# Kernel tuning notes

Hardware: AMD Instinct MI355X
Metric: run time of the kernel (lower is better)

Reference implementation:

```python
import jax, jax.numpy as jnp
import numpy as np

N_NODES = 50000
BN_EPS = 1e-5
L2_EPS = 1e-12


def setup_inputs() -> dict:
    key = jax.random.key(0)
    k_h, k_w, k_s, k_d = jax.random.split(key, 4)
    h = jax.random.normal(k_h, (N_NODES, 128), dtype=jnp.float32)
    W = jax.random.normal(k_w, (128, 128), dtype=jnp.float32) * (1.0 / np.sqrt(128))
    gamma = jnp.ones((128,), dtype=jnp.float32)
    beta = jnp.zeros((128,), dtype=jnp.float32)
    src = jax.random.randint(k_s, (600000,), 0, N_NODES, dtype=jnp.int64 if jax.config.jax_enable_x64 else jnp.int32)
    dst = jax.random.randint(k_d, (600000,), 0, N_NODES, dtype=jnp.int64 if jax.config.jax_enable_x64 else jnp.int32)
    return {"h": h, "W": W, "gamma": gamma, "beta": beta, "src": src, "dst": dst}


def reference(h, W, gamma, beta, src, dst):
    N = h.shape[0]
    ones = jnp.ones(src.shape[0], dtype=h.dtype)
    # degrees, clamped to >= 1 (DGL GraphConv norm='both')
    deg_out = jnp.clip(jax.ops.segment_sum(ones, src, num_segments=N), 1.0)
    deg_in = jnp.clip(jax.ops.segment_sum(ones, dst, num_segments=N), 1.0)
    # src-side normalization
    hn = h * jax.lax.rsqrt(deg_out)[:, None]
    # gather-scatter aggregation over edges (sum of src messages at dst)
    agg = jax.ops.segment_sum(hn[src], dst, num_segments=N)  # [N, dim_in]
    # dst-side normalization, then linear (in_feats <= out_feats branch)
    agg = agg * jax.lax.rsqrt(deg_in)[:, None]
    out = agg @ W  # [N, dim_out]
    # BatchNorm1d (training-mode batch stats, biased variance)
    mu = jnp.mean(out, axis=0)
    var = jnp.mean(jnp.square(out - mu), axis=0)
    out = (out - mu) * jax.lax.rsqrt(var + BN_EPS) * gamma + beta
    # ReLU
    out = jax.nn.relu(out)
    # F.normalize(p=2, dim=1)
    norm = jnp.sqrt(jnp.sum(jnp.square(out), axis=1, keepdims=True))
    out = out / jnp.maximum(norm, L2_EPS)
    return out
```

## Files before the change

### kernel.cpp

```cpp
#include <hip/hip_runtime.h>
#include <hip/hip_bf16.h>

#define N_NODES 50000
#define N_EDGES 600000
#define SLOTS 64
#define GEMM_BLOCKS 782
#define GATHER_BLOCKS 3125
#define NPART 3125
#define RED_BLOCKS 125

#define Z_OFF        0ull
#define ESRCP_OFF    12800000ull
#define CURS_OFF     25600000ull
#define DEGO_OFF     25800000ull
#define ZERO_OFF     25600000ull
#define ZERO_BYTES   400000ull
#define FLAG_OFF     26000064ull
#define WSW_OFF      26000128ull
#define PSUM_OFF     26032896ull
#define PSQ_OFF      27632896ull
#define PS2_OFF      29232896ull
#define PQ2_OFF      29296896ull
#define SCALE_OFF    29360896ull
#define SHIFT_OFF    29361408ull
#define OUTPRE_OFF   33554432ull
#define HN_OFF       46354432ull

typedef short bf16x8 __attribute__((ext_vector_type(8)));
typedef float f32x4  __attribute__((ext_vector_type(4)));

__device__ __forceinline__ float bf16lo(unsigned int v) { return __uint_as_float(v << 16); }
__device__ __forceinline__ float bf16hi(unsigned int v) { return __uint_as_float(v & 0xffff0000u); }
__device__ __forceinline__ unsigned int packbf16(float x, float y) {
  union { __hip_bfloat162 v; unsigned int u; } cvt;
  cvt.v.x = __float2bfloat16(x);
  cvt.v.y = __float2bfloat16(y);
  return cvt.u;
}

__global__ __launch_bounds__(256) void k_build(const int* __restrict__ src,
                                               const int* __restrict__ dst,
                                               int* __restrict__ cursor,
                                               int* __restrict__ dego,
                                               int* __restrict__ esrcPad,
                                               const unsigned int* __restrict__ hu,
                                               int* __restrict__ flag) {
  __shared__ int cnt;
  if (blockIdx.x == 0) {
    if (threadIdx.x == 0) cnt = 0;
    __syncthreads();
    unsigned int u = hu[threadIdx.x];
    int ex = (u >> 7) & 0xFF;
    if (ex >= 100 && ex <= 140) atomicAdd(&cnt, 1);
    __syncthreads();
    if (threadIdx.x == 0) *flag = (cnt >= 128) ? 1 : 0;
  }
  int e = blockIdx.x * 256 + threadIdx.x;
  if (e < N_EDGES) {
    int s = src[e];
    int d = dst[e];
    atomicAdd(&dego[s], 1);
    int slot = atomicAdd(&cursor[d], 1);
    if (slot < SLOTS) esrcPad[d * SLOTS + slot] = s;
  }
}

__global__ __launch_bounds__(256) void k_prep(const void* __restrict__ hraw,
                                              const int* __restrict__ dego,
                                              const int* __restrict__ flag,
                                              unsigned int* __restrict__ hn,
                                              const void* __restrict__ Wraw,
                                              unsigned int* __restrict__ wsw) {
  int isbf = *flag;
  if (blockIdx.x < 32) {
    int i = blockIdx.x * 256 + threadIdx.x;
    int tileIdx = i >> 8;
    int rem     = i & 255;
    int ln      = rem >> 2;
    int dw      = rem & 3;
    int kb      = tileIdx & 3;
    int ct      = tileIdx >> 2;
    int q       = ln >> 4;
    int n       = ln & 15;
    int k       = kb * 32 + q * 8 + dw * 2;
    int c       = ct * 16 + n;
    unsigned int val;
    if (isbf) {
      const unsigned int* Wd = (const unsigned int*)Wraw;
      unsigned int u0 = Wd[k * 64 + (c >> 1)];
      unsigned int u1 = Wd[(k + 1) * 64 + (c >> 1)];
      unsigned int h0 = (c & 1) ? (u0 >> 16) : (u0 & 0xffffu);
      unsigned int h1 = (c & 1) ? (u1 >> 16) : (u1 & 0xffffu);
      val = h0 | (h1 << 16);
    } else {
      const float* Wf = (const float*)Wraw;
      val = packbf16(Wf[k * 128 + c], Wf[(k + 1) * 128 + c]);
    }
    wsw[i] = val;
  }
  int nn = blockIdx.x * 4 + (threadIdx.x >> 6);
  int l = threadIdx.x & 63;
  float c = rsqrtf((float)max(dego[nn], 1));
  unsigned int out;
  if (isbf) {
    unsigned int v = ((const unsigned int*)hraw)[(size_t)nn * 64 + l];
    out = packbf16(bf16lo(v) * c, bf16hi(v) * c);
  } else {
    float2 v = ((const float2*)hraw)[(size_t)nn * 64 + l];
    out = packbf16(v.x * c, v.y * c);
  }
  hn[(size_t)nn * 64 + l] = out;
}

__global__ __launch_bounds__(256) void k_gemmZ(const unsigned int* __restrict__ hn,
                                               const unsigned int* __restrict__ wsw,
                                               __hip_bfloat16* __restrict__ Z) {
  __shared__ uint4 lb4[2048];
  __shared__ unsigned int la[64 * 68];
  unsigned int* lb = (unsigned int*)lb4;
  int t = threadIdx.x;
  int r0 = blockIdx.x * 64;

  for (int i = t; i < 2048; i += 256) lb4[i] = ((const uint4*)wsw)[i];
  for (int i = t; i < 1024; i += 256) {
    int row  = i >> 4;
    int dpos = (i & 15) * 4;
    int r    = r0 + row;
    uint4 v;
    if (r < N_NODES) v = *(const uint4*)&hn[(size_t)r * 64 + dpos];
    else             v = make_uint4(0u, 0u, 0u, 0u);
    *(uint4*)&la[row * 68 + dpos] = v;
  }
  __syncthreads();

  int l = t & 63;
  int w = t >> 6;
  int m = l & 15;
  int q = l >> 4;

  f32x4 acc[8];
#pragma unroll
  for (int ct = 0; ct < 8; ++ct) acc[ct] = (f32x4){0.f, 0.f, 0.f, 0.f};

#pragma unroll
  for (int kb = 0; kb < 4; ++kb) {
    bf16x8 af = *(const bf16x8*)&la[(w * 16 + m) * 68 + kb * 16 + q * 4];
#pragma unroll
    for (int ct = 0; ct < 8; ++ct) {
      bf16x8 bfv = *(const bf16x8*)&lb[(ct * 4 + kb) * 256 + l * 4];
      acc[ct] = __builtin_amdgcn_mfma_f32_16x16x32_bf16(af, bfv, acc[ct], 0, 0, 0);
    }
  }

#pragma unroll
  for (int ct = 0; ct < 8; ++ct) {
    int col = ct * 16 + m;
#pragma unroll
    for (int reg = 0; reg < 4; ++reg) {
      int row = r0 + w * 16 + q * 4 + reg;
      if (row < N_NODES) Z[(size_t)row * 128 + col] = __float2bfloat16(acc[ct][reg]);
    }
  }
}

__global__ __launch_bounds__(256) void k_gatherZ(const unsigned int* __restrict__ Zd,
                                                 const int* __restrict__ cursor,
                                                 const int* __restrict__ esrcPad,
                                                 unsigned int* __restrict__ outpre,
                                                 float* __restrict__ psum,
                                                 float* __restrict__ psq) {
  __shared__ float sred[4 * 128];
  int t = threadIdx.x;
  int w = t >> 6;
  int l = t & 63;
  float s1a = 0.f, s1b = 0.f, s2a = 0.f, s2b = 0.f;
#pragma unroll
  for (int i = 0; i < 4; ++i) {
    int n = blockIdx.x * 16 + w * 4 + i;
    int di = cursor[n];
    int cnt = di < SLOTS ? di : SLOTS;
    const int* row = esrcPad + n * SLOTS;
    float a0 = 0.f, a1 = 0.f;
    int j = 0;
    for (; j + 3 < cnt; j += 4) {
      int4 s4 = *(const int4*)&row[j];
      unsigned int v0 = Zd[(size_t)s4.x * 64 + l];
      unsigned int v1 = Zd[(size_t)s4.y * 64 + l];
      unsigned int v2 = Zd[(size_t)s4.z * 64 + l];
      unsigned int v3 = Zd[(size_t)s4.w * 64 + l];
      a0 += bf16lo(v0) + bf16lo(v1) + bf16lo(v2) + bf16lo(v3);
      a1 += bf16hi(v0) + bf16hi(v1) + bf16hi(v2) + bf16hi(v3);
    }
    for (; j < cnt; ++j) {
      unsigned int v = Zd[(size_t)row[j] * 64 + l];
      a0 += bf16lo(v);
      a1 += bf16hi(v);
    }
    float scn = rsqrtf((float)(di < 1 ? 1 : di));
    a0 *= scn; a1 *= scn;
    outpre[(size_t)n * 64 + l] = packbf16(a0, a1);
    s1a += a0; s2a += a0 * a0;
    s1b += a1; s2b += a1 * a1;
  }
  sred[w * 128 + 2 * l]     = s1a;
  sred[w * 128 + 2 * l + 1] = s1b;
  __syncthreads();
  if (t < 128) {
    float v = sred[t] + sred[128 + t] + sred[256 + t] + sred[384 + t];
    psum[(size_t)blockIdx.x * 128 + t] = v;
  }
  __syncthreads();
  sred[w * 128 + 2 * l]     = s2a;
  sred[w * 128 + 2 * l + 1] = s2b;
  __syncthreads();
  if (t < 128) {
    float v = sred[t] + sred[128 + t] + sred[256 + t] + sred[384 + t];
    psq[(size_t)blockIdx.x * 128 + t] = v;
  }
}

__global__ __launch_bounds__(256) void k_bnred(const float* __restrict__ psum,
                                               const float* __restrict__ psq,
                                               float* __restrict__ ps2,
                                               float* __restrict__ pq2) {
  __shared__ float r1[256], r2[256];
  int t = threadIdx.x;
  int c = t & 127;
  int j = t >> 7;
  int b0 = blockIdx.x * 25;
  float s1 = 0.f, s2 = 0.f;
  for (int b = b0 + j; b < b0 + 25; b += 2) {
    s1 += psum[(size_t)b * 128 + c];
    s2 += psq [(size_t)b * 128 + c];
  }
  r1[t] = s1; r2[t] = s2;
  __syncthreads();
  if (j == 0) {
    ps2[(size_t)blockIdx.x * 128 + c] = s1 + r1[c + 128];
    pq2[(size_t)blockIdx.x * 128 + c] = s2 + r2[c + 128];
  }
}

__global__ __launch_bounds__(1024) void k_bnfinal(const float* __restrict__ ps2,
                                                  const float* __restrict__ pq2,
                                                  const void* __restrict__ gamma,
                                                  const void* __restrict__ beta,
                                                  const int* __restrict__ flag,
                                                  float* __restrict__ scale,
                                                  float* __restrict__ shift) {
  __shared__ float r1[1024], r2[1024];
  int t = threadIdx.x;
  int c = t & 127;
  int j = t >> 7;
  float s1 = 0.f, s2 = 0.f;
  for (int b = j; b < RED_BLOCKS; b += 8) {
    s1 += ps2[(size_t)b * 128 + c];
    s2 += pq2[(size_t)b * 128 + c];
  }
  r1[t] = s1; r2[t] = s2;
  __syncthreads();
  if (j == 0) {
#pragma unroll
    for (int jj = 1; jj < 8; ++jj) { s1 += r1[c + 128 * jj]; s2 += r2[c + 128 * jj]; }
    const float invN = 1.0f / (float)N_NODES;
    float mu  = s1 * invN;
    float var = s2 * invN - mu * mu;
    float is  = rsqrtf(var + 1e-5f);
    float g, b;
    if (*flag) {
      g = __bfloat162float(((const __hip_bfloat16*)gamma)[c]);
      b = __bfloat162float(((const __hip_bfloat16*)beta)[c]);
    } else {
      g = ((const float*)gamma)[c];
      b = ((const float*)beta)[c];
    }
    scale[c] = g * is;
    shift[c] = b - mu * g * is;
  }
}

__global__ __launch_bounds__(256) void k_rownorm(const unsigned int* __restrict__ outpre,
                                                 const float* __restrict__ scale,
                                                 const float* __restrict__ shift,
                                                 const int* __restrict__ flag,
                                                 void* __restrict__ outraw) {
  int r = blockIdx.x * 4 + (threadIdx.x >> 6);
  int l = threadIdx.x & 63;
  unsigned int xv = outpre[(size_t)r * 64 + l];
  float2 sc = *(const float2*)&scale[2 * l];
  float2 sh = *(const float2*)&shift[2 * l];
  float y0 = fmaxf(bf16lo(xv) * sc.x + sh.x, 0.f);
  float y1 = fmaxf(bf16hi(xv) * sc.y + sh.y, 0.f);
  float ss = y0 * y0 + y1 * y1;
#pragma unroll
  for (int o = 1; o < 64; o <<= 1) ss += __shfl_xor(ss, o, 64);
  float inv = 1.0f / fmaxf(sqrtf(ss), 1e-12f);
  y0 *= inv; y1 *= inv;
  if (*flag) {
    ((unsigned int*)outraw)[(size_t)r * 64 + l] = packbf16(y0, y1);
  } else {
    float2 o2; o2.x = y0; o2.y = y1;
    ((float2*)outraw)[(size_t)r * 64 + l] = o2;
  }
}

extern "C" void kernel_launch(void* const* d_in, const int* in_sizes, int n_in,
                              void* d_out, int out_size, void* d_ws, size_t ws_size,
                              hipStream_t stream) {
  const void* h     = d_in[0];
  const void* W     = d_in[1];
  const void* gamma = d_in[2];
  const void* beta  = d_in[3];
  const int*  src   = (const int*)d_in[4];
  const int*  dst   = (const int*)d_in[5];

  char* ws = (char*)d_ws;
  unsigned int* Zd   = (unsigned int*)(ws + Z_OFF);
  int*   esrcPad = (int*)(ws + ESRCP_OFF);
  int*   cursor  = (int*)(ws + CURS_OFF);
  int*   dego    = (int*)(ws + DEGO_OFF);
  int*   flag    = (int*)(ws + FLAG_OFF);
  unsigned int* wsw = (unsigned int*)(ws + WSW_OFF);
  float* psum    = (float*)(ws + PSUM_OFF);
  float* psq     = (float*)(ws + PSQ_OFF);
  float* ps2     = (float*)(ws + PS2_OFF);
  float* pq2     = (float*)(ws + PQ2_OFF);
  float* scale   = (float*)(ws + SCALE_OFF);
  float* shift   = (float*)(ws + SHIFT_OFF);
  unsigned int* outpre = (unsigned int*)(ws + OUTPRE_OFF);
  unsigned int* hn     = (unsigned int*)(ws + HN_OFF);

  (void)hipMemsetAsync(ws + ZERO_OFF, 0, ZERO_BYTES, stream);

  hipLaunchKernelGGL(k_build, dim3((N_EDGES + 255) / 256), dim3(256), 0, stream,
                     src, dst, cursor, dego, esrcPad, (const unsigned int*)h, flag);
  hipLaunchKernelGGL(k_prep, dim3(N_NODES / 4), dim3(256), 0, stream,
                     h, dego, flag, hn, W, wsw);
  hipLaunchKernelGGL(k_gemmZ, dim3(GEMM_BLOCKS), dim3(256), 0, stream,
                     hn, wsw, (__hip_bfloat16*)Zd);
  hipLaunchKernelGGL(k_gatherZ, dim3(GATHER_BLOCKS), dim3(256), 0, stream,
                     Zd, cursor, esrcPad, outpre, psum, psq);
  hipLaunchKernelGGL(k_bnred, dim3(RED_BLOCKS), dim3(256), 0, stream,
                     psum, psq, ps2, pq2);
  hipLaunchKernelGGL(k_bnfinal, dim3(1), dim3(1024), 0, stream,
                     ps2, pq2, gamma, beta, flag, scale, shift);
  hipLaunchKernelGGL(k_rownorm, dim3(N_NODES / 4), dim3(256), 0, stream,
                     outpre, scale, shift, flag, (unsigned int*)d_out);
}
```

Measured before the change: 216.4 us.

## Fuse prep into build and GEMM, move BN partial stats into reduction kernel

The W swizzle moves into extra blocks of the edge-build kernel, and the degree scaling and bf16 conversion of h move into the GEMM's tile load, so the separate prep kernel and the hn buffer go away. The gather kernel no longer computes per-block BN partial sums. Instead k_bnred reads the bf16 outpre back and reduces it per 400-row chunk. This saves one launch and the hn write/read, at the cost of re-reading outpre (about 12.8MB) for the statistics. The stats are now computed from bf16-rounded values, a small precision change.

```diff
diff --git a/kernel.cpp b/kernel.cpp
--- a/kernel.cpp
+++ b/kernel.cpp
@@ -4,9 +4,9 @@
 #define N_NODES 50000
 #define N_EDGES 600000
 #define SLOTS 64
+#define EDGE_BLOCKS 2344
 #define GEMM_BLOCKS 782
 #define GATHER_BLOCKS 3125
-#define NPART 3125
 #define RED_BLOCKS 125
 
 #define Z_OFF        0ull
@@ -17,14 +17,11 @@
 #define ZERO_BYTES   400000ull
 #define FLAG_OFF     26000064ull
 #define WSW_OFF      26000128ull
-#define PSUM_OFF     26032896ull
-#define PSQ_OFF      27632896ull
-#define PS2_OFF      29232896ull
-#define PQ2_OFF      29296896ull
-#define SCALE_OFF    29360896ull
-#define SHIFT_OFF    29361408ull
+#define PS2_OFF      26032896ull
+#define PQ2_OFF      26096896ull
+#define SCALE_OFF    26160896ull
+#define SHIFT_OFF    26161408ull
 #define OUTPRE_OFF   33554432ull
-#define HN_OFF       46354432ull
 
 typedef short bf16x8 __attribute__((ext_vector_type(8)));
 typedef float f32x4  __attribute__((ext_vector_type(4)));
@@ -44,36 +41,20 @@
                                                int* __restrict__ dego,
                                                int* __restrict__ esrcPad,
                                                const unsigned int* __restrict__ hu,
-                                               int* __restrict__ flag) {
-  __shared__ int cnt;
-  if (blockIdx.x == 0) {
-    if (threadIdx.x == 0) cnt = 0;
+                                               int* __restrict__ flag,
+                                               const void* __restrict__ Wraw,
+                                               unsigned int* __restrict__ wsw) {
+  int t = threadIdx.x;
+  if (blockIdx.x >= EDGE_BLOCKS) {
+    __shared__ int cnt;
+    if (t == 0) cnt = 0;
     __syncthreads();
-    unsigned int u = hu[threadIdx.x];
+    unsigned int u = hu[t];
     int ex = (u >> 7) & 0xFF;
     if (ex >= 100 && ex <= 140) atomicAdd(&cnt, 1);
     __syncthreads();
-    if (threadIdx.x == 0) *flag = (cnt >= 128) ? 1 : 0;
-  }
-  int e = blockIdx.x * 256 + threadIdx.x;
-  if (e < N_EDGES) {
-    int s = src[e];
-    int d = dst[e];
-    atomicAdd(&dego[s], 1);
-    int slot = atomicAdd(&cursor[d], 1);
-    if (slot < SLOTS) esrcPad[d * SLOTS + slot] = s;
-  }
-}
-
-__global__ __launch_bounds__(256) void k_prep(const void* __restrict__ hraw,
-                                              const int* __restrict__ dego,
-                                              const int* __restrict__ flag,
-                                              unsigned int* __restrict__ hn,
-                                              const void* __restrict__ Wraw,
-                                              unsigned int* __restrict__ wsw) {
-  int isbf = *flag;
-  if (blockIdx.x < 32) {
-    int i = blockIdx.x * 256 + threadIdx.x;
+    int isbf = (cnt >= 128);
+    int i = (blockIdx.x - EDGE_BLOCKS) * 256 + t;
     int tileIdx = i >> 8;
     int rem     = i & 255;
     int ln      = rem >> 2;
@@ -97,22 +78,31 @@
       val = packbf16(Wf[k * 128 + c], Wf[(k + 1) * 128 + c]);
     }
     wsw[i] = val;
-  }
-  int nn = blockIdx.x * 4 + (threadIdx.x >> 6);
-  int l = threadIdx.x & 63;
-  float c = rsqrtf((float)max(dego[nn], 1));
-  unsigned int out;
-  if (isbf) {
-    unsigned int v = ((const unsigned int*)hraw)[(size_t)nn * 64 + l];
-    out = packbf16(bf16lo(v) * c, bf16hi(v) * c);
-  } else {
-    float2 v = ((const float2*)hraw)[(size_t)nn * 64 + l];
-    out = packbf16(v.x * c, v.y * c);
-  }
-  hn[(size_t)nn * 64 + l] = out;
-}
-
-__global__ __launch_bounds__(256) void k_gemmZ(const unsigned int* __restrict__ hn,
+    return;
+  }
+  if (blockIdx.x == 0) {
+    __shared__ int cnt0;
+    if (t == 0) cnt0 = 0;
+    __syncthreads();
+    unsigned int u = hu[t];
+    int ex = (u >> 7) & 0xFF;
+    if (ex >= 100 && ex <= 140) atomicAdd(&cnt0, 1);
+    __syncthreads();
+    if (t == 0) *flag = (cnt0 >= 128) ? 1 : 0;
+  }
+  int e = blockIdx.x * 256 + t;
+  if (e < N_EDGES) {
+    int s = src[e];
+    int d = dst[e];
+    atomicAdd(&dego[s], 1);
+    int slot = atomicAdd(&cursor[d], 1);
+    if (slot < SLOTS) esrcPad[d * SLOTS + slot] = s;
+  }
+}
+
+__global__ __launch_bounds__(256) void k_gemmZ(const void* __restrict__ hraw,
+                                               const int* __restrict__ dego,
+                                               const int* __restrict__ flag,
                                                const unsigned int* __restrict__ wsw,
                                                __hip_bfloat16* __restrict__ Z) {
   __shared__ uint4 lb4[2048];
@@ -120,16 +110,34 @@
   unsigned int* lb = (unsigned int*)lb4;
   int t = threadIdx.x;
   int r0 = blockIdx.x * 64;
+  int isbf = *flag;
 
   for (int i = t; i < 2048; i += 256) lb4[i] = ((const uint4*)wsw)[i];
   for (int i = t; i < 1024; i += 256) {
     int row  = i >> 4;
     int dpos = (i & 15) * 4;
     int r    = r0 + row;
-    uint4 v;
-    if (r < N_NODES) v = *(const uint4*)&hn[(size_t)r * 64 + dpos];
-    else             v = make_uint4(0u, 0u, 0u, 0u);
-    *(uint4*)&la[row * 68 + dpos] = v;
+    unsigned int o0 = 0, o1 = 0, o2 = 0, o3 = 0;
+    if (r < N_NODES) {
+      float c = rsqrtf((float)max(dego[r], 1));
+      if (isbf) {
+        uint4 v = *(const uint4*)&((const unsigned int*)hraw)[(size_t)r * 64 + dpos];
+        o0 = packbf16(bf16lo(v.x) * c, bf16hi(v.x) * c);
+        o1 = packbf16(bf16lo(v.y) * c, bf16hi(v.y) * c);
+        o2 = packbf16(bf16lo(v.z) * c, bf16hi(v.z) * c);
+        o3 = packbf16(bf16lo(v.w) * c, bf16hi(v.w) * c);
+      } else {
+        const float* hF = (const float*)hraw;
+        float4 a = *(const float4*)&hF[(size_t)r * 128 + dpos * 2];
+        float4 b = *(const float4*)&hF[(size_t)r * 128 + dpos * 2 + 4];
+        o0 = packbf16(a.x * c, a.y * c);
+        o1 = packbf16(a.z * c, a.w * c);
+        o2 = packbf16(b.x * c, b.y * c);
+        o3 = packbf16(b.z * c, b.w * c);
+      }
+    }
+    unsigned int* p = &la[row * 68 + dpos];
+    p[0] = o0; p[1] = o1; p[2] = o2; p[3] = o3;
   }
   __syncthreads();
 
@@ -166,14 +174,10 @@
 __global__ __launch_bounds__(256) void k_gatherZ(const unsigned int* __restrict__ Zd,
                                                  const int* __restrict__ cursor,
                                                  const int* __restrict__ esrcPad,
-                                                 unsigned int* __restrict__ outpre,
-                                                 float* __restrict__ psum,
-                                                 float* __restrict__ psq) {
-  __shared__ float sred[4 * 128];
+                                                 unsigned int* __restrict__ outpre) {
   int t = threadIdx.x;
   int w = t >> 6;
   int l = t & 63;
-  float s1a = 0.f, s1b = 0.f, s2a = 0.f, s2b = 0.f;
 #pragma unroll
   for (int i = 0; i < 4; ++i) {
     int n = blockIdx.x * 16 + w * 4 + i;
@@ -197,47 +201,37 @@
       a1 += bf16hi(v);
     }
     float scn = rsqrtf((float)(di < 1 ? 1 : di));
-    a0 *= scn; a1 *= scn;
-    outpre[(size_t)n * 64 + l] = packbf16(a0, a1);
-    s1a += a0; s2a += a0 * a0;
-    s1b += a1; s2b += a1 * a1;
+    outpre[(size_t)n * 64 + l] = packbf16(a0 * scn, a1 * scn);
+  }
+}
+
+__global__ __launch_bounds__(256) void k_bnred(const unsigned int* __restrict__ outpre,
+                                               float* __restrict__ ps2,
+                                               float* __restrict__ pq2) {
+  __shared__ float sred[4 * 128];
+  int t = threadIdx.x;
+  int w = t >> 6;
+  int l = t & 63;
+  int r0 = blockIdx.x * 400;
+  float s1a = 0.f, s1b = 0.f, s2a = 0.f, s2b = 0.f;
+  for (int r = r0 + w; r < r0 + 400; r += 4) {
+    unsigned int v = outpre[(size_t)r * 64 + l];
+    float x0 = bf16lo(v), x1 = bf16hi(v);
+    s1a += x0; s2a += x0 * x0;
+    s1b += x1; s2b += x1 * x1;
   }
   sred[w * 128 + 2 * l]     = s1a;
   sred[w * 128 + 2 * l + 1] = s1b;
   __syncthreads();
   if (t < 128) {
-    float v = sred[t] + sred[128 + t] + sred[256 + t] + sred[384 + t];
-    psum[(size_t)blockIdx.x * 128 + t] = v;
+    ps2[(size_t)blockIdx.x * 128 + t] = sred[t] + sred[128 + t] + sred[256 + t] + sred[384 + t];
   }
   __syncthreads();
   sred[w * 128 + 2 * l]     = s2a;
   sred[w * 128 + 2 * l + 1] = s2b;
   __syncthreads();
   if (t < 128) {
-    float v = sred[t] + sred[128 + t] + sred[256 + t] + sred[384 + t];
-    psq[(size_t)blockIdx.x * 128 + t] = v;
-  }
-}
-
-__global__ __launch_bounds__(256) void k_bnred(const float* __restrict__ psum,
-                                               const float* __restrict__ psq,
-                                               float* __restrict__ ps2,
-                                               float* __restrict__ pq2) {
-  __shared__ float r1[256], r2[256];
-  int t = threadIdx.x;
-  int c = t & 127;
-  int j = t >> 7;
-  int b0 = blockIdx.x * 25;
-  float s1 = 0.f, s2 = 0.f;
-  for (int b = b0 + j; b < b0 + 25; b += 2) {
-    s1 += psum[(size_t)b * 128 + c];
-    s2 += psq [(size_t)b * 128 + c];
-  }
-  r1[t] = s1; r2[t] = s2;
-  __syncthreads();
-  if (j == 0) {
-    ps2[(size_t)blockIdx.x * 128 + c] = s1 + r1[c + 128];
-    pq2[(size_t)blockIdx.x * 128 + c] = s2 + r2[c + 128];
+    pq2[(size_t)blockIdx.x * 128 + t] = sred[t] + sred[128 + t] + sred[256 + t] + sred[384 + t];
   }
 }
 
@@ -321,27 +315,22 @@
   int*   dego    = (int*)(ws + DEGO_OFF);
   int*   flag    = (int*)(ws + FLAG_OFF);
   unsigned int* wsw = (unsigned int*)(ws + WSW_OFF);
-  float* psum    = (float*)(ws + PSUM_OFF);
-  float* psq     = (float*)(ws + PSQ_OFF);
   float* ps2     = (float*)(ws + PS2_OFF);
   float* pq2     = (float*)(ws + PQ2_OFF);
   float* scale   = (float*)(ws + SCALE_OFF);
   float* shift   = (float*)(ws + SHIFT_OFF);
   unsigned int* outpre = (unsigned int*)(ws + OUTPRE_OFF);
-  unsigned int* hn     = (unsigned int*)(ws + HN_OFF);
 
   (void)hipMemsetAsync(ws + ZERO_OFF, 0, ZERO_BYTES, stream);
 
-  hipLaunchKernelGGL(k_build, dim3((N_EDGES + 255) / 256), dim3(256), 0, stream,
-                     src, dst, cursor, dego, esrcPad, (const unsigned int*)h, flag);
-  hipLaunchKernelGGL(k_prep, dim3(N_NODES / 4), dim3(256), 0, stream,
-                     h, dego, flag, hn, W, wsw);
+  hipLaunchKernelGGL(k_build, dim3(EDGE_BLOCKS + 32), dim3(256), 0, stream,
+                     src, dst, cursor, dego, esrcPad, (const unsigned int*)h, flag, W, wsw);
   hipLaunchKernelGGL(k_gemmZ, dim3(GEMM_BLOCKS), dim3(256), 0, stream,
-                     hn, wsw, (__hip_bfloat16*)Zd);
+                     h, dego, flag, wsw, (__hip_bfloat16*)Zd);
   hipLaunchKernelGGL(k_gatherZ, dim3(GATHER_BLOCKS), dim3(256), 0, stream,
-                     Zd, cursor, esrcPad, outpre, psum, psq);
+                     Zd, cursor, esrcPad, outpre);
   hipLaunchKernelGGL(k_bnred, dim3(RED_BLOCKS), dim3(256), 0, stream,
-                     psum, psq, ps2, pq2);
+                     outpre, ps2, pq2);
   hipLaunchKernelGGL(k_bnfinal, dim3(1), dim3(1024), 0, stream,
                      ps2, pq2, gamma, beta, flag, scale, shift);
   hipLaunchKernelGGL(k_rownorm, dim3(N_NODES / 4), dim3(256), 0, stream,
```

After: 220.9 us. 2.1% more time.
